# Kernel tuning notes

Measured on AMD Instinct MI355X. Metric: run time of the kernel, lower is better.

## Reference

```python
import jax, jax.numpy as jnp
import numpy as np

# NSA hyperparams (match init_kwargs)
KS, ST, SEL, TOPN, WIN = 32, 16, 64, 16, 512
NEG = -1e30  # additive mask value (finite so fp32 softmax stays stable)


def setup_inputs() -> dict:
    key = jax.random.key(0)
    ks = jax.random.split(key, 6)
    B, S, Hq, Hk, D, Dv = 1, 2048, 16, 2, 128, 128
    q = jax.random.normal(ks[0], (B, S, Hq, D), jnp.float32)
    k = jax.random.normal(ks[1], (B, S, Hk, D), jnp.float32)
    v = jax.random.normal(ks[2], (B, S, Hk, Dv), jnp.float32)
    # learned per-position compression weights for K and V blocks
    w_cmp_k = jax.random.normal(ks[3], (KS,), jnp.float32) / KS
    w_cmp_v = jax.random.normal(ks[4], (KS,), jnp.float32) / KS
    # gating head: Linear(qk_head_dim, 3) -> sigmoid
    w_gate = jax.random.normal(ks[5], (D, 3), jnp.float32) * 0.02
    b_gate = jnp.zeros((3,), jnp.float32)
    return dict(q=q, k=k, v=v, w_cmp_k=w_cmp_k, w_cmp_v=w_cmp_v,
                w_gate=w_gate, b_gate=b_gate)


def _nsa(q, k, v, w_cmp_k, w_cmp_v, w_gate, b_gate):
    B, S, Hq, D = q.shape
    Hk = k.shape[2]
    G = Hq // Hk                      # GQA group size
    Dv = v.shape[-1]
    scale = D ** -0.5
    t_pos = jnp.arange(S)

    # ---- 1. compressed-KV attention (CompressAttn) ----
    T = (S - KS) // ST + 1            # number of compressed blocks
    widx = jnp.arange(T)[:, None] * ST + jnp.arange(KS)[None, :]   # [T, KS]
    cmp_k = jnp.einsum('btknd,k->btnd', k[:, widx], w_cmp_k)        # [B,T,Hk,D]
    cmp_v = jnp.einsum('btknd,k->btnd', v[:, widx], w_cmp_v)        # [B,T,Hk,Dv]

    qg = q.reshape(B, S, Hk, G, D)
    s_cmp = jnp.einsum('bsngd,btnd->bngst', qg, cmp_k) * scale      # [B,Hk,G,S,T]
    blk_end = jnp.arange(T) * ST + KS - 1
    cmp_mask = blk_end[None, :] <= t_pos[:, None]                   # [S,T] block fully past
    p_cmp = jax.nn.softmax(jnp.where(cmp_mask, s_cmp, NEG), axis=-1)
    p_cmp = p_cmp * cmp_mask          # zero rows with no visible block
    cmp_o = jnp.einsum('bngst,btnd->bsngd', p_cmp, cmp_v).reshape(B, S, Hq, Dv)

    # ---- 2. top-n selection-block scoring (select_for_fwd_bwd) ----
    NSel = S // SEL
    starts = jnp.arange(T) * ST
    b_lo = starts // SEL
    b_hi = (starts + KS - 1) // SEL
    bidx = jnp.arange(NSel)
    # map compressed-block probs onto overlapping selection blocks
    Mmap = ((bidx[None, :] >= b_lo[:, None]) & (bidx[None, :] <= b_hi[:, None])).astype(q.dtype)  # [T,NSel]
    p_slc = jnp.einsum('bngst,tm->bnsm', p_cmp, Mmap)               # sum over group g -> [B,Hk,S,NSel]

    cur_blk = t_pos // SEL
    blk_causal = (bidx[None, :] * SEL) <= t_pos[:, None]            # [S,NSel]
    forced = (bidx[None, :] == 0) | (bidx[None, :] == cur_blk[:, None])
    blk_score = jnp.where(forced, -NEG, p_slc)                      # always keep block 0 + current
    blk_score = jnp.where(blk_causal, blk_score, NEG)
    vals, inds = jax.lax.top_k(blk_score, TOPN)                     # [B,Hk,S,TOPN]
    valid = (vals > NEG / 2).astype(q.dtype)
    sel_blk_mask = (jax.nn.one_hot(inds, NSel, dtype=q.dtype) * valid[..., None]).sum(-2) > 0  # [B,Hk,S,NSel]

    # ---- 3. block-sparse selected attention (select_attn) ----
    tok_sel_mask = jnp.repeat(sel_blk_mask, SEL, axis=-1)           # [B,Hk,S,S]
    causal = t_pos[None, :] <= t_pos[:, None]                       # [S,S]
    tok_sel_mask = tok_sel_mask & causal
    s_tok = jnp.einsum('bsngd,bjnd->bngsj', qg, k) * scale          # [B,Hk,G,S,S] shared scores
    p_sel = jax.nn.softmax(jnp.where(tok_sel_mask[:, :, None], s_tok, NEG), axis=-1)
    sel_o = jnp.einsum('bngsj,bjnd->bsngd', p_sel, v).reshape(B, S, Hq, Dv)

    win_mask = causal & ((t_pos[:, None] - t_pos[None, :]) <= WIN)
    p_win = jax.nn.softmax(jnp.where(win_mask, s_tok, NEG), axis=-1)
    win_o = jnp.einsum('bngsj,bjnd->bsngd', p_win, v).reshape(B, S, Hq, Dv)

    # ---- 5. learned sigmoid gating combine ----
    gate = jax.nn.sigmoid(jnp.einsum('bshd,dc->bshc', q, w_gate) + b_gate)  # [B,S,Hq,3]
    return (cmp_o * gate[..., 0:1] + sel_o * gate[..., 1:2] + win_o * gate[..., 2:3])


def reference(q, k, v, w_cmp_k, w_cmp_v, w_gate, b_gate):
    return _nsa(q, k, v, w_cmp_k, w_cmp_v, w_gate, b_gate)
```

## Files before the change

kernel.cpp:

```cpp
#include <hip/hip_runtime.h>

#define SS   2048
#define HQ   16
#define HK   2
#define GQ   8
#define DD   128
#define DV   128
#define KS   32
#define ST   16
#define SELB 64
#define TOPN 16
#define WINW 512
#define TT   127
#define NSEL 32
#define SCALE 0.08838834764831845f

typedef __attribute__((ext_vector_type(8))) short bf16x8;
typedef __attribute__((ext_vector_type(4))) short short4v;
typedef __attribute__((ext_vector_type(4))) float f32x4;

__device__ __forceinline__ short f2bf(float x) {
    union { float f; unsigned u; } a; a.f = x;
    unsigned r = a.u + 0x7FFFu + ((a.u >> 16) & 1u);
    return (short)(r >> 16);
}
__device__ __forceinline__ float bf2f(short b) {
    union { unsigned u; float f; } x; x.u = ((unsigned)(unsigned short)b) << 16; return x.f;
}

__global__ __launch_bounds__(256) void k_prep(
    const float* __restrict__ k, const float* __restrict__ v,
    const float* __restrict__ wck, const float* __restrict__ wcv,
    short* __restrict__ kfr, short* __restrict__ vfr,
    short* __restrict__ ckh, short* __restrict__ ckl,
    short* __restrict__ cvfr)
{
    int bid = blockIdx.x, tid = threadIdx.x;
    int lane = tid & 63, quad = (lane >> 4) & 3, l16 = lane & 15;
    if (bid < 256) {
        int tb = bid >> 1, n = bid & 1;
        int kb = tid >> 6;
        int token = tb * 16 + l16;
        int feat = kb * 32 + quad * 8;
        const float* src = &k[(token * HK + n) * DD + feat];
        bf16x8 t;
        #pragma unroll
        for (int e = 0; e < 8; ++e) t[e] = f2bf(src[e]);
        *(bf16x8*)&kfr[(((n * 128 + tb) * 4 + kb) * 64 + lane) * 8] = t;
    } else if (bid < 320) {
        int id = bid - 256;
        int cb = id >> 1, n = id & 1;
        #pragma unroll
        for (int it = 0; it < 4; ++it) {
            int frag = it * 4 + (tid >> 6);
            int h = frag >> 3, f = frag & 7;
            int d = f * 16 + l16;
            int tok0 = cb * 64 + h * 32 + quad * 8;
            bf16x8 t;
            #pragma unroll
            for (int e = 0; e < 8; ++e) t[e] = f2bf(v[((tok0 + e) * HK + n) * DV + d]);
            *(bf16x8*)&vfr[((((n * 32 + cb) * 2 + h) * 8 + f) * 64 + lane) * 8] = t;
        }
    } else if (bid < 576) {
        int id = bid - 320;
        int n = id & 1, t = id >> 1;
        if (tid < 128) {
            int d = tid;
            float a = 0.f;
            if (t < TT) {
                for (int j = 0; j < KS; ++j)
                    a += k[((t * ST + j) * HK + n) * DD + d] * wck[j];
            }
            short hi = f2bf(a);
            short lo = f2bf(a - bf2f(hi));
            int tile = t >> 4, l16i = t & 15;
            int kb = d >> 5, qd = (d >> 3) & 3, e = d & 7;
            int off = (((n * 8 + tile) * 4 + kb) * 64 + qd * 16 + l16i) * 8 + e;
            ckh[off] = hi;
            ckl[off] = lo;
        }
    } else {
        int id = bid - 576;
        int n = id & 1, tok = id >> 1;
        if (tid < 128) {
            int d = tid;
            float a = 0.f;
            if (tok < TT) {
                for (int j = 0; j < KS; ++j)
                    a += v[((tok * ST + j) * HK + n) * DV + d] * wcv[j];
            }
            int w2 = d >> 5, half = (d >> 4) & 1, l16i = d & 15;
            int kb = tok >> 5, qd = (tok >> 3) & 3, e = tok & 7;
            cvfr[((((n * 4 + w2) * 2 + half) * 4 + kb) * 64 + qd * 16 + l16i) * 8 + e] = f2bf(a);
        }
    }
}

__global__ __launch_bounds__(256, 4) void k_fused(
    const float* __restrict__ q,
    const short* __restrict__ ckh, const short* __restrict__ ckl,
    const short* __restrict__ cvfr,
    const short* __restrict__ kfr, const short* __restrict__ vfr,
    const float* __restrict__ wg, const float* __restrict__ bg,
    float* __restrict__ out)
{
    int s0 = (SS - 2) - (int)blockIdx.x * 2;
    int s1 = s0 + 1;
    int n = blockIdx.y;
    int tid = threadIdx.x;
    int w = tid >> 6, lane = tid & 63, quad = lane >> 4, l16 = lane & 15;

    __shared__ union {
        struct {
            float qs[16][132];
            float p[16][128];
            short Pt[16][136];
        } c;
        union {
            short Pw[4][16][72];
            float o_lds[2][16][132];
        } f;
    } u;
    __shared__ short cmpO[16][136];
    __shared__ short OselB[16][128];
    __shared__ float g3v[16][3];
    __shared__ float pslc2[2][NSEL];
    __shared__ float lw[4][16];
    __shared__ unsigned selMask[2];
    __shared__ unsigned ublk[NSEL];
    __shared__ int shUCnt;

    f32x4 z4 = {0.f, 0.f, 0.f, 0.f};

    for (int i = tid; i < 16 * 128; i += 256) {
        int row = i >> 7, d = i & 127;
        u.c.qs[row][d] = q[((s0 + (row >> 3)) * HQ + n * GQ + (row & 7)) * DD + d];
    }
    __syncthreads();

    bf16x8 qb[4];
    bf16x8 qlb[4];
    {
        const float* qp = &u.c.qs[l16][quad * 8];
        #pragma unroll
        for (int kb = 0; kb < 4; ++kb) {
            f32x4 x = *(const f32x4*)(qp + kb * 32);
            f32x4 y = *(const f32x4*)(qp + kb * 32 + 4);
            bf16x8 th, tl;
            #pragma unroll
            for (int j = 0; j < 4; ++j) {
                th[j] = f2bf(x[j]);     tl[j] = f2bf(x[j] - bf2f(th[j]));
                th[4+j] = f2bf(y[j]);   tl[4+j] = f2bf(y[j] - bf2f(th[4+j]));
            }
            qb[kb] = th; qlb[kb] = tl;
        }
    }
    if (tid < 48) {
        int h2 = tid / 3, c = tid % 3;
        float a = 0.f;
        for (int d2 = 0; d2 < DD; ++d2) a += u.c.qs[h2][d2] * wg[d2 * 3 + c];
        a += bg[c];
        g3v[h2][c] = 1.f / (1.f + __expf(-a));
    }
    for (int tile = w; tile < 8; tile += 4) {
        const short* khp = &ckh[((n * 8 + tile) * 256 + lane) * 8];
        const short* klp = &ckl[((n * 8 + tile) * 256 + lane) * 8];
        f32x4 acc = z4;
        #pragma unroll
        for (int kb = 0; kb < 4; ++kb) {
            bf16x8 ah = *(const bf16x8*)(khp + kb * 512);
            bf16x8 al = *(const bf16x8*)(klp + kb * 512);
            acc = __builtin_amdgcn_mfma_f32_16x16x32_bf16(ah, qb[kb], acc, 0, 0, 0);
            acc = __builtin_amdgcn_mfma_f32_16x16x32_bf16(al, qb[kb], acc, 0, 0, 0);
            acc = __builtin_amdgcn_mfma_f32_16x16x32_bf16(ah, qlb[kb], acc, 0, 0, 0);
        }
        f32x4 sv;
        #pragma unroll
        for (int r = 0; r < 4; ++r) sv[r] = acc[r] * SCALE;
        *(f32x4*)&u.c.p[l16][tile * 16 + quad * 4] = sv;
    }
    __syncthreads();

    int ntt0 = (s0 >= KS - 1) ? min((s0 - (KS - 1)) / ST + 1, TT) : 0;
    int ntt1 = (s1 >= KS - 1) ? min((s1 - (KS - 1)) / ST + 1, TT) : 0;

    #pragma unroll
    for (int rr = 0; rr < 4; ++rr) {
        int row = w * 4 + rr;
        int ntt = (row < 8) ? ntt0 : ntt1;
        int t1 = lane, t2 = lane + 64;
        float v1 = (t1 < ntt) ? u.c.p[row][t1] : -1e30f;
        float v2 = (t2 < ntt) ? u.c.p[row][t2] : -1e30f;
        float m = fmaxf(v1, v2);
        #pragma unroll
        for (int o = 32; o > 0; o >>= 1) m = fmaxf(m, __shfl_xor(m, o, 64));
        float e1 = (t1 < ntt) ? __expf(v1 - m) : 0.f;
        float e2 = (t2 < ntt) ? __expf(v2 - m) : 0.f;
        float ssum = e1 + e2;
        #pragma unroll
        for (int o = 32; o > 0; o >>= 1) ssum += __shfl_xor(ssum, o, 64);
        float inv = (ntt > 0) ? (1.f / ssum) : 0.f;
        e1 *= inv; e2 *= inv;
        u.c.p[row][t1] = e1; u.c.p[row][t2] = e2;
        u.c.Pt[row][t1] = f2bf(e1); u.c.Pt[row][t2] = f2bf(e2);
    }
    __syncthreads();

    if (tid < 64) {
        int p01 = tid >> 5, m = tid & 31;
        float a = 0.f;
        for (int dt = -1; dt < 4; ++dt) {
            int t = 4 * m + dt;
            if (t < 0 || t >= TT) continue;
            bool maps = (t / 4 == m) || ((t % 4 == 3) && (t / 4 == m - 1));
            if (!maps) continue;
            for (int g = 0; g < GQ; ++g) a += u.c.p[p01 * 8 + g][t];
        }
        pslc2[p01][m] = a;
    }
    __syncthreads();

    if (w < 2) {
        int p01 = w;
        int sp = p01 ? s1 : s0;
        int cur = sp / SELB;
        float v;
        if (lane < NSEL) {
            int m = lane;
            if (m == 0 || m == cur) v = 1e30f;
            else if (m * SELB <= sp) v = pslc2[p01][m];
            else v = -1e30f;
        } else v = -1e31f;
        unsigned msk = 0;
        #pragma unroll
        for (int pick = 0; pick < TOPN; ++pick) {
            float bv = v;
            #pragma unroll
            for (int o = 32; o > 0; o >>= 1) bv = fmaxf(bv, __shfl_xor(bv, o, 64));
            unsigned long long b = __ballot(v == bv);
            int best = __ffsll((long long)b) - 1;
            if (bv > -5e29f) msk |= 1u << best;
            if (lane == best) v = -1e31f;
        }
        if (lane == 0) selMask[p01] = msk;
    }
    {
        f32x4 o0 = z4, o1 = z4;
        int d0 = w * 32 + l16;
        const short* cvp = &cvfr[((n * 4 + w) * 512 + lane) * 8];
        #pragma unroll
        for (int kb = 0; kb < 4; ++kb) {
            bf16x8 pa = *(const bf16x8*)&u.c.Pt[l16][kb * 32 + quad * 8];
            bf16x8 vb0 = *(const bf16x8*)(cvp + kb * 512);
            bf16x8 vb1 = *(const bf16x8*)(cvp + 2048 + kb * 512);
            o0 = __builtin_amdgcn_mfma_f32_16x16x32_bf16(pa, vb0, o0, 0, 0, 0);
            o1 = __builtin_amdgcn_mfma_f32_16x16x32_bf16(pa, vb1, o1, 0, 0, 0);
        }
        #pragma unroll
        for (int r = 0; r < 4; ++r) {
            int h2 = quad * 4 + r;
            cmpO[h2][d0]      = f2bf(o0[r]);
            cmpO[h2][d0 + 16] = f2bf(o1[r]);
        }
    }
    __syncthreads();

    if (tid == 0) {
        unsigned m0 = selMask[0], m1 = selMask[1], mu = m0 | m1;
        int uc = 0;
        for (int b = 0; b < NSEL; ++b)
            if ((mu >> b) & 1u)
                ublk[uc++] = (unsigned)(b * SELB) | (((m0 >> b) & 1u) << 30) | (((m1 >> b) & 1u) << 31);
        shUCnt = uc;
    }
    __syncthreads();
    int uCnt = shUCnt;
    int j00 = (s0 >= WINW) ? (s0 - WINW) : 0;
    int j01 = (s1 >= WINW) ? (s1 - WINW) : 0;
    int tb0 = j00 & ~63;
    int nBlkB = ((s1 - tb0) >> 6) + 1;

    int sLim = (l16 < 8) ? s0 : s1;
    f32x4 o[8];
    float lold;

    auto run_chunks = [&](int nB, bool selMode) {
        #pragma unroll
        for (int f = 0; f < 8; ++f) o[f] = z4;
        lold = 0.f;
        int loWin = selMode ? 0 : ((l16 < 8) ? j00 : j01);
        for (int bi = w; bi < nB; bi += 4) {
            int tstart, vis;
            if (selMode) {
                unsigned e = ublk[bi];
                tstart = (int)(e & 0x0FFFFFFFu);
                vis = (l16 < 8) ? (int)((e >> 30) & 1u) : (int)(e >> 31);
            } else {
                tstart = tb0 + bi * 64;
                vis = 1;
            }
            f32x4 a4[4] = {z4, z4, z4, z4};
            {
                const short* kp = &kfr[((n * 128 + (tstart >> 4)) * 256 + lane) * 8];
                bf16x8 kf[2][4];
                #pragma unroll
                for (int t2 = 0; t2 < 2; ++t2)
                    #pragma unroll
                    for (int kb = 0; kb < 4; ++kb)
                        kf[t2][kb] = *(const bf16x8*)(kp + (t2 * 4 + kb) * 512);
                #pragma unroll
                for (int kb = 0; kb < 4; ++kb) {
                    a4[0] = __builtin_amdgcn_mfma_f32_16x16x32_bf16(kf[0][kb], qb[kb], a4[0], 0, 0, 0);
                    a4[1] = __builtin_amdgcn_mfma_f32_16x16x32_bf16(kf[1][kb], qb[kb], a4[1], 0, 0, 0);
                }
                #pragma unroll
                for (int t2 = 0; t2 < 2; ++t2)
                    #pragma unroll
                    for (int kb = 0; kb < 4; ++kb)
                        kf[t2][kb] = *(const bf16x8*)(kp + ((2 + t2) * 4 + kb) * 512);
                #pragma unroll
                for (int kb = 0; kb < 4; ++kb) {
                    a4[2] = __builtin_amdgcn_mfma_f32_16x16x32_bf16(kf[0][kb], qb[kb], a4[2], 0, 0, 0);
                    a4[3] = __builtin_amdgcn_mfma_f32_16x16x32_bf16(kf[1][kb], qb[kb], a4[3], 0, 0, 0);
                }
            }
            const short* vp = &vfr[((n * 32 + (tstart >> 6)) * 1024 + lane) * 8];
            bf16x8 vf[8];
            #pragma unroll
            for (int f = 0; f < 8; ++f) vf[f] = *(const bf16x8*)(vp + f * 512);
            {
                int lo = loWin - tstart;
                int hi = vis ? (sLim - tstart) : (lo - 1);
                int rngS = hi - lo + 1;
                unsigned rng = (unsigned)(rngS > 0 ? rngS : 0);
                int tb = quad * 4 - lo;
                #pragma unroll
                for (int tile = 0; tile < 4; ++tile) {
                    float ev[4];
                    #pragma unroll
                    for (int r = 0; r < 4; ++r) {
                        unsigned uu = (unsigned)(tb + tile * 16 + r);
                        float ex = __expf(a4[tile][r] * SCALE);
                        ev[r] = (uu < rng) ? ex : 0.f;
                    }
                    lold += (ev[0] + ev[1]) + (ev[2] + ev[3]);
                    unsigned plo = (__float_as_uint(ev[1]) & 0xFFFF0000u) | (__float_as_uint(ev[0]) >> 16);
                    unsigned phi = (__float_as_uint(ev[3]) & 0xFFFF0000u) | (__float_as_uint(ev[2]) >> 16);
                    uint2 pk; pk.x = plo; pk.y = phi;
                    *(uint2*)&u.f.Pw[w][l16][tile * 16 + quad * 4] = pk;
                }
            }
            __builtin_amdgcn_s_waitcnt(0xC07F);
            bf16x8 pa0 = *(const bf16x8*)&u.f.Pw[w][l16][quad * 8];
            bf16x8 pa1 = *(const bf16x8*)&u.f.Pw[w][l16][32 + quad * 8];
            #pragma unroll
            for (int f = 0; f < 8; ++f)
                o[f] = __builtin_amdgcn_mfma_f32_16x16x32_bf16(pa0, vf[f], o[f], 0, 0, 0);
            #pragma unroll
            for (int f = 0; f < 8; ++f)
                o[f] = __builtin_amdgcn_mfma_f32_16x16x32_bf16(pa1, *(const bf16x8*)(vp + (8 + f) * 512), o[f], 0, 0, 0);
        }
    };

    auto combine = [&](bool isA) {
        float lsum = lold;
        lsum += __shfl_xor(lsum, 16, 64);
        lsum += __shfl_xor(lsum, 32, 64);
        if (quad == 0) lw[w][l16] = lsum;
        __syncthreads();
        if (w >= 2) {
            #pragma unroll
            for (int f = 0; f < 8; ++f)
                #pragma unroll
                for (int r = 0; r < 4; ++r)
                    u.f.o_lds[w - 2][quad * 4 + r][l16 + 16 * f] = o[f][r];
        }
        __syncthreads();
        float ltot = lw[0][l16] + lw[1][l16] + lw[2][l16] + lw[3][l16];
        float linv = 1.f / ltot;
        float linvr[4];
        #pragma unroll
        for (int r = 0; r < 4; ++r) linvr[r] = __shfl(linv, quad * 4 + r, 64);
        if (w < 2) {
            #pragma unroll
            for (int f = 0; f < 8; ++f)
                #pragma unroll
                for (int r = 0; r < 4; ++r)
                    o[f][r] += u.f.o_lds[w][quad * 4 + r][l16 + 16 * f];
        }
        __syncthreads();
        if (w == 1) {
            #pragma unroll
            for (int f = 0; f < 8; ++f)
                #pragma unroll
                for (int r = 0; r < 4; ++r)
                    u.f.o_lds[0][quad * 4 + r][l16 + 16 * f] = o[f][r];
        }
        __syncthreads();
        if (w == 0) {
            #pragma unroll
            for (int f = 0; f < 8; ++f)
                #pragma unroll
                for (int r = 0; r < 4; ++r)
                    o[f][r] += u.f.o_lds[0][quad * 4 + r][l16 + 16 * f];
            if (isA) {
                #pragma unroll
                for (int f = 0; f < 8; ++f)
                    #pragma unroll
                    for (int r = 0; r < 4; ++r)
                        OselB[quad * 4 + r][l16 + 16 * f] = f2bf(o[f][r] * linvr[r]);
            } else {
                #pragma unroll
                for (int f = 0; f < 8; ++f)
                    #pragma unroll
                    for (int r = 0; r < 4; ++r) {
                        int h2 = quad * 4 + r;
                        int p = h2 >> 3, g = h2 & 7;
                        int d = l16 + 16 * f;
                        int ob = ((s0 + p) * HQ + n * GQ + g) * DV + d;
                        float owin = o[f][r] * linvr[r];
                        out[ob] = g3v[h2][0] * bf2f(cmpO[h2][d]) + g3v[h2][1] * bf2f(OselB[h2][d]) + g3v[h2][2] * owin;
                    }
            }
        }
        __syncthreads();
    };

    run_chunks(uCnt, true);
    combine(true);
    run_chunks(nBlkB, false);
    combine(false);
}

extern "C" void kernel_launch(void* const* d_in, const int* in_sizes, int n_in,
                              void* d_out, int out_size, void* d_ws, size_t ws_size,
                              hipStream_t stream) {
    const float* q   = (const float*)d_in[0];
    const float* k   = (const float*)d_in[1];
    const float* v   = (const float*)d_in[2];
    const float* wck = (const float*)d_in[3];
    const float* wcv = (const float*)d_in[4];
    const float* wg  = (const float*)d_in[5];
    const float* bg  = (const float*)d_in[6];
    float* out = (float*)d_out;

    short* kfr  = (short*)d_ws;
    short* vfr  = kfr + 2 * 128 * 4 * 64 * 8;
    short* ckh  = vfr + 2 * 32 * 2 * 8 * 64 * 8;
    short* ckl  = ckh + 2 * 8 * 4 * 64 * 8;
    short* cvfr = ckl + 2 * 8 * 4 * 64 * 8;

    k_prep<<<832, 256, 0, stream>>>(k, v, wck, wcv, kfr, vfr, ckh, ckl, cvfr);
    k_fused<<<dim3(SS / 2, HK), 256, 0, stream>>>(q, ckh, ckl, cvfr, kfr, vfr, wg, bg, out);
}
```

Baseline: 170.2 us.

## Swizzle P tile in LDS, shrink shared footprint, parallelize prep kernel

In the fused kernel, the per-wave P staging buffer loses its padding and switches to an XOR-swizzled 16-byte chunk layout, so reads and writes avoid LDS bank conflicts. OselB moves into the union with the other buffers to cut total LDS use, which could raise occupancy. The prep kernel splits V fragment conversion across four times as many blocks and uses all 256 threads for the compressed K/V reductions, with an LDS add of two halves. The extra syncthreads and larger grid add a little overhead in the prep kernel.

Measured after the change: 170.9 us. Within noise of the previous version (+0.4%).

```diff
diff --git a/kernel.cpp b/kernel.cpp
--- a/kernel.cpp
+++ b/kernel.cpp
@@ -35,6 +35,7 @@
     short* __restrict__ ckh, short* __restrict__ ckl,
     short* __restrict__ cvfr)
 {
+    __shared__ float red[256];
     int bid = blockIdx.x, tid = threadIdx.x;
     int lane = tid & 63, quad = (lane >> 4) & 3, l16 = lane & 15;
     if (bid < 256) {
@@ -47,32 +48,35 @@
         #pragma unroll
         for (int e = 0; e < 8; ++e) t[e] = f2bf(src[e]);
         *(bf16x8*)&kfr[(((n * 128 + tb) * 4 + kb) * 64 + lane) * 8] = t;
-    } else if (bid < 320) {
+    } else if (bid < 512) {
         int id = bid - 256;
-        int cb = id >> 1, n = id & 1;
-        #pragma unroll
-        for (int it = 0; it < 4; ++it) {
-            int frag = it * 4 + (tid >> 6);
-            int h = frag >> 3, f = frag & 7;
-            int d = f * 16 + l16;
-            int tok0 = cb * 64 + h * 32 + quad * 8;
-            bf16x8 t;
-            #pragma unroll
-            for (int e = 0; e < 8; ++e) t[e] = f2bf(v[((tok0 + e) * HK + n) * DV + d]);
-            *(bf16x8*)&vfr[((((n * 32 + cb) * 2 + h) * 8 + f) * 64 + lane) * 8] = t;
-        }
-    } else if (bid < 576) {
-        int id = bid - 320;
+        int cb = id >> 3, n = (id >> 2) & 1, it = id & 3;
+        int frag = it * 4 + (tid >> 6);
+        int h = frag >> 3, f = frag & 7;
+        int d = f * 16 + l16;
+        int tok0 = cb * 64 + h * 32 + quad * 8;
+        bf16x8 t;
+        #pragma unroll
+        for (int e = 0; e < 8; ++e) t[e] = f2bf(v[((tok0 + e) * HK + n) * DV + d]);
+        *(bf16x8*)&vfr[((((n * 32 + cb) * 2 + h) * 8 + f) * 64 + lane) * 8] = t;
+    } else if (bid < 768) {
+        int id = bid - 512;
         int n = id & 1, t = id >> 1;
+        int d = tid & 127, jh = tid >> 7;
+        float a = 0.f;
+        if (t < TT) {
+            #pragma unroll
+            for (int jj = 0; jj < 16; ++jj) {
+                int j = jh * 16 + jj;
+                a += k[((t * ST + j) * HK + n) * DD + d] * wck[j];
+            }
+        }
+        red[tid] = a;
+        __syncthreads();
         if (tid < 128) {
-            int d = tid;
-            float a = 0.f;
-            if (t < TT) {
-                for (int j = 0; j < KS; ++j)
-                    a += k[((t * ST + j) * HK + n) * DD + d] * wck[j];
-            }
-            short hi = f2bf(a);
-            short lo = f2bf(a - bf2f(hi));
+            float s = red[tid] + red[tid + 128];
+            short hi = f2bf(s);
+            short lo = f2bf(s - bf2f(hi));
             int tile = t >> 4, l16i = t & 15;
             int kb = d >> 5, qd = (d >> 3) & 3, e = d & 7;
             int off = (((n * 8 + tile) * 4 + kb) * 64 + qd * 16 + l16i) * 8 + e;
@@ -80,18 +84,24 @@
             ckl[off] = lo;
         }
     } else {
-        int id = bid - 576;
+        int id = bid - 768;
         int n = id & 1, tok = id >> 1;
+        int d = tid & 127, jh = tid >> 7;
+        float a = 0.f;
+        if (tok < TT) {
+            #pragma unroll
+            for (int jj = 0; jj < 16; ++jj) {
+                int j = jh * 16 + jj;
+                a += v[((tok * ST + j) * HK + n) * DV + d] * wcv[j];
+            }
+        }
+        red[tid] = a;
+        __syncthreads();
         if (tid < 128) {
-            int d = tid;
-            float a = 0.f;
-            if (tok < TT) {
-                for (int j = 0; j < KS; ++j)
-                    a += v[((tok * ST + j) * HK + n) * DV + d] * wcv[j];
-            }
+            float s = red[tid] + red[tid + 128];
             int w2 = d >> 5, half = (d >> 4) & 1, l16i = d & 15;
             int kb = tok >> 5, qd = (tok >> 3) & 3, e = tok & 7;
-            cvfr[((((n * 4 + w2) * 2 + half) * 4 + kb) * 64 + qd * 16 + l16i) * 8 + e] = f2bf(a);
+            cvfr[((((n * 4 + w2) * 2 + half) * 4 + kb) * 64 + qd * 16 + l16i) * 8 + e] = f2bf(s);
         }
     }
 }
@@ -113,16 +123,18 @@
     __shared__ union {
         struct {
             float qs[16][132];
-            float p[16][128];
+            float p[16][132];
             short Pt[16][136];
         } c;
-        union {
-            short Pw[4][16][72];
-            float o_lds[2][16][132];
+        struct {
+            union {
+                short Pw[4][16][64];
+                float o_lds[2][16][132];
+            } pf;
+            short OselB[16][128];
         } f;
     } u;
     __shared__ short cmpO[16][136];
-    __shared__ short OselB[16][128];
     __shared__ float g3v[16][3];
     __shared__ float pslc2[2][NSEL];
     __shared__ float lw[4][16];
@@ -284,6 +296,9 @@
     f32x4 o[8];
     float lold;
 
+    char* pwRow = (char*)&u.f.pf.Pw[w][l16][0];
+    int swz = l16 & 7;
+
     auto run_chunks = [&](int nB, bool selMode) {
         #pragma unroll
         for (int f = 0; f < 8; ++f) o[f] = z4;
@@ -347,12 +362,13 @@
                     unsigned plo = (__float_as_uint(ev[1]) & 0xFFFF0000u) | (__float_as_uint(ev[0]) >> 16);
                     unsigned phi = (__float_as_uint(ev[3]) & 0xFFFF0000u) | (__float_as_uint(ev[2]) >> 16);
                     uint2 pk; pk.x = plo; pk.y = phi;
-                    *(uint2*)&u.f.Pw[w][l16][tile * 16 + quad * 4] = pk;
+                    int chunk = (tile * 2 + (quad >> 1)) ^ swz;
+                    *(uint2*)(pwRow + chunk * 16 + (quad & 1) * 8) = pk;
                 }
             }
             __builtin_amdgcn_s_waitcnt(0xC07F);
-            bf16x8 pa0 = *(const bf16x8*)&u.f.Pw[w][l16][quad * 8];
-            bf16x8 pa1 = *(const bf16x8*)&u.f.Pw[w][l16][32 + quad * 8];
+            bf16x8 pa0 = *(const bf16x8*)(pwRow + ((quad ^ swz) * 16));
+            bf16x8 pa1 = *(const bf16x8*)(pwRow + (((4 + quad) ^ swz) * 16));
             #pragma unroll
             for (int f = 0; f < 8; ++f)
                 o[f] = __builtin_amdgcn_mfma_f32_16x16x32_bf16(pa0, vf[f], o[f], 0, 0, 0);
@@ -373,7 +389,7 @@
             for (int f = 0; f < 8; ++f)
                 #pragma unroll
                 for (int r = 0; r < 4; ++r)
-                    u.f.o_lds[w - 2][quad * 4 + r][l16 + 16 * f] = o[f][r];
+                    u.f.pf.o_lds[w - 2][quad * 4 + r][l16 + 16 * f] = o[f][r];
         }
         __syncthreads();
         float ltot = lw[0][l16] + lw[1][l16] + lw[2][l16] + lw[3][l16];
@@ -386,7 +402,7 @@
             for (int f = 0; f < 8; ++f)
                 #pragma unroll
                 for (int r = 0; r < 4; ++r)
-                    o[f][r] += u.f.o_lds[w][quad * 4 + r][l16 + 16 * f];
+                    o[f][r] += u.f.pf.o_lds[w][quad * 4 + r][l16 + 16 * f];
         }
         __syncthreads();
         if (w == 1) {
@@ -394,7 +410,7 @@
             for (int f = 0; f < 8; ++f)
                 #pragma unroll
                 for (int r = 0; r < 4; ++r)
-                    u.f.o_lds[0][quad * 4 + r][l16 + 16 * f] = o[f][r];
+                    u.f.pf.o_lds[0][quad * 4 + r][l16 + 16 * f] = o[f][r];
         }
         __syncthreads();
         if (w == 0) {
@@ -402,13 +418,13 @@
             for (int f = 0; f < 8; ++f)
                 #pragma unroll
                 for (int r = 0; r < 4; ++r)
-                    o[f][r] += u.f.o_lds[0][quad * 4 + r][l16 + 16 * f];
+                    o[f][r] += u.f.pf.o_lds[0][quad * 4 + r][l16 + 16 * f];
             if (isA) {
                 #pragma unroll
                 for (int f = 0; f < 8; ++f)
                     #pragma unroll
                     for (int r = 0; r < 4; ++r)
-                        OselB[quad * 4 + r][l16 + 16 * f] = f2bf(o[f][r] * linvr[r]);
+                        u.f.OselB[quad * 4 + r][l16 + 16 * f] = f2bf(o[f][r] * linvr[r]);
             } else {
                 #pragma unroll
                 for (int f = 0; f < 8; ++f)
@@ -419,7 +435,7 @@
                         int d = l16 + 16 * f;
                         int ob = ((s0 + p) * HQ + n * GQ + g) * DV + d;
                         float owin = o[f][r] * linvr[r];
-                        out[ob] = g3v[h2][0] * bf2f(cmpO[h2][d]) + g3v[h2][1] * bf2f(OselB[h2][d]) + g3v[h2][2] * owin;
+                        out[ob] = g3v[h2][0] * bf2f(cmpO[h2][d]) + g3v[h2][1] * bf2f(u.f.OselB[h2][d]) + g3v[h2][2] * owin;
                     }
             }
         }
@@ -450,6 +466,6 @@
     short* ckl  = ckh + 2 * 8 * 4 * 64 * 8;
     short* cvfr = ckl + 2 * 8 * 4 * 64 * 8;
 
-    k_prep<<<832, 256, 0, stream>>>(k, v, wck, wcv, kfr, vfr, ckh, ckl, cvfr);
+    k_prep<<<1024, 256, 0, stream>>>(k, v, wck, wcv, kfr, vfr, ckh, ckl, cvfr);
     k_fused<<<dim3(SS / 2, HK), 256, 0, stream>>>(q, ckh, ckl, cvfr, kfr, vfr, wg, bg, out);
 }
```
